# Kernel optimization log

Hardware: AMD Instinct MI355X
Metric: run time of the kernel (lower is better)

Reference implementation:

```python
import jax, jax.numpy as jnp
import numpy as np

N = 100_000   # nodes
E = 1_250_000 # edges
D = 64        # feature dim


def setup_inputs() -> dict:
    key = jax.random.key(0)
    k1, k2, k3, k4 = jax.random.split(key, 4)
    x = jax.random.normal(k1, (N, D), dtype=jnp.float32)
    edge_index = jax.random.randint(k2, (2, E), 0, N, dtype=jnp.int32)
    s = 1.0 / np.sqrt(D)  # glorot-ish scale
    W1 = jax.random.uniform(k3, (D, D), minval=-s, maxval=s, dtype=jnp.float32)
    W2 = jax.random.uniform(k4, (D, D), minval=-s, maxval=s, dtype=jnp.float32)
    b1 = jnp.zeros((D,), jnp.float32)
    b2 = jnp.zeros((D,), jnp.float32)
    return {"x": x, "edge_index": edge_index, "W1": W1, "b1": b1, "W2": W2, "b2": b2}


def gcn_conv(x, edge_index, W, b):
    # PyG GCNConv: add self-loops, symmetric normalization D^-1/2 A D^-1/2,
    # linear transform, scatter-add aggregation over destination nodes.
    n = x.shape[0]
    src, dst = edge_index[0], edge_index[1]
    xw = x @ W  # [N, D]
    deg = jax.ops.segment_sum(jnp.ones((edge_index.shape[1],), x.dtype), dst,
                              num_segments=n) + 1.0  # +1 for self-loop
    inv_sqrt = jax.lax.rsqrt(deg)  # [N]
    coef = inv_sqrt[src] * inv_sqrt[dst]  # [E]
    agg = jax.ops.segment_sum(xw[src] * coef[:, None], dst, num_segments=n)
    # self-loop contribution: coef_ii = deg_i^-1
    agg = agg + xw * (inv_sqrt * inv_sqrt)[:, None]
    return agg + b


def reference(x, edge_index, W1, b1, W2, b2):
    h = jax.nn.relu(gcn_conv(x, edge_index, W1, b1))
    # dropout p=0.6 is identity in eval mode (training=False)
    out = gcn_conv(h, edge_index, W2, b2)
    return jax.nn.log_softmax(out, axis=1)
```

## Files before the change

kernel.cpp:

```cpp
#include <hip/hip_runtime.h>

#define DD 64
#define BSH 8
#define NB_MAX 512
#define SCAP 4096
#define BIN_CH 4096

typedef __attribute__((ext_vector_type(8))) short bf16x8;
typedef __attribute__((ext_vector_type(4))) float f32x4;
union Frag { bf16x8 v; uint32_t d[4]; };

__device__ __forceinline__ float bf_lo(uint32_t d) { return __uint_as_float(d << 16); }
__device__ __forceinline__ float bf_hi(uint32_t d) { return __uint_as_float(d & 0xffff0000u); }
__device__ __forceinline__ float bf2f(uint32_t h) { return __uint_as_float(h << 16); }
__device__ __forceinline__ uint32_t f2bf(float f) {
    uint32_t u = __float_as_uint(f);
    u += 0x7fffu + ((u >> 16) & 1u);
    return u >> 16;
}

__global__ __launch_bounds__(256) void bin_kernel(const int* __restrict__ src,
                                                  const int* __restrict__ dst,
                                                  int* __restrict__ bcnt,
                                                  uint32_t* __restrict__ staging,
                                                  int E, int NB) {
    __shared__ uint32_t cnt[NB_MAX];
    __shared__ uint32_t resv[NB_MAX];
    __shared__ uint16_t rk[BIN_CH];
    int tid = threadIdx.x;
    int base = blockIdx.x * BIN_CH;
    for (int b = tid; b < NB; b += 256) cnt[b] = 0;
    __syncthreads();
    for (int k = tid; k < BIN_CH; k += 256) {
        int g = base + k;
        if (g < E) {
            int b = dst[g] >> BSH;
            rk[k] = (uint16_t)atomicAdd(&cnt[b], 1u);
        }
    }
    __syncthreads();
    for (int b = tid; b < NB; b += 256) {
        uint32_t c = cnt[b];
        resv[b] = c ? (uint32_t)atomicAdd(&bcnt[b], (int)c) : 0u;
    }
    __syncthreads();
    for (int k = tid; k < BIN_CH; k += 256) {
        int g = base + k;
        if (g < E) {
            int s = src[g], d = dst[g];
            int b = d >> BSH;
            uint32_t pos = resv[b] + rk[k];
            if (pos < SCAP)
                staging[(size_t)b * SCAP + pos] = ((uint32_t)s << BSH) | (uint32_t)(d & ((1 << BSH) - 1));
        }
    }
}

__global__ __launch_bounds__(256) void sort_kernel(const int* __restrict__ bcnt,
                                                   const uint32_t* __restrict__ staging,
                                                   int* __restrict__ rowptr,
                                                   float* __restrict__ inv,
                                                   uint32_t* __restrict__ srcs,
                                                   int n, int E, int NB) {
    __shared__ uint32_t raw[SCAP];
    __shared__ uint32_t sorted[SCAP];
    __shared__ int scnt[1 << BSH];
    __shared__ int soff[1 << BSH];
    __shared__ int lcur[1 << BSH];
    __shared__ int red[256];
    int tid = threadIdx.x;
    int b = blockIdx.x;
    int base = b << BSH;
    int nd = min(1 << BSH, n - base);
    int cb = min(bcnt[b], SCAP);

    int part = 0;
    for (int j = tid; j < b; j += 256) part += bcnt[j];
    red[tid] = part;
    __syncthreads();
    for (int o = 128; o > 0; o >>= 1) {
        if (tid < o) red[tid] += red[tid + o];
        __syncthreads();
    }
    int bbase = red[0];

    scnt[tid] = 0;
    if (tid < ((1 << BSH) - 256)) {}
    __syncthreads();
    for (int k = tid; k < cb; k += 256) {
        uint32_t w = staging[(size_t)b * SCAP + k];
        raw[k] = w;
        atomicAdd(&scnt[w & ((1 << BSH) - 1)], 1);
    }
    __syncthreads();
    int v = scnt[tid];
    red[tid] = v;
    __syncthreads();
    for (int o = 1; o < 256; o <<= 1) {
        int t = (tid >= o) ? red[tid - o] : 0;
        __syncthreads();
        red[tid] += t;
        __syncthreads();
    }
    soff[tid] = red[tid] - v;
    lcur[tid] = red[tid] - v;
    if (tid < nd) {
        rowptr[base + tid] = bbase + soff[tid];
        inv[base + tid] = rsqrtf((float)v + 1.0f);
    }
    if (b == NB - 1 && tid == 0) rowptr[n] = E;
    __syncthreads();
    for (int k = tid; k < cb; k += 256) {
        uint32_t w = raw[k];
        int p = atomicAdd(&lcur[w & ((1 << BSH) - 1)], 1);
        sorted[p] = w >> BSH;
    }
    __syncthreads();
    for (int k = tid; k < cb; k += 256) srcs[bbase + k] = sorted[k];
}

template <int XBF>
__global__ __launch_bounds__(256) void gemm64_mfma(const void* __restrict__ Xv,
                                                   const float* __restrict__ W,
                                                   uint16_t* __restrict__ Y, int n) {
    __shared__ float Ws[DD * DD];
    int tid = threadIdx.x;
    for (int i = tid; i < DD * DD; i += 256) Ws[i] = W[i];
    __syncthreads();
    int lane = tid & 63, quad = lane >> 4, l16 = lane & 15;

    Frag bhi[4][2], blo[4][2];
#pragma unroll
    for (int t = 0; t < 4; ++t)
#pragma unroll
        for (int c = 0; c < 2; ++c) {
            int col = t * 16 + l16;
            int kb = c * 32 + quad * 8;
#pragma unroll
            for (int i = 0; i < 4; ++i) {
                float w0 = Ws[(kb + 2 * i) * DD + col];
                float w1 = Ws[(kb + 2 * i + 1) * DD + col];
                uint32_t h0 = f2bf(w0), h1 = f2bf(w1);
                uint32_t l0 = f2bf(w0 - bf2f(h0)), l1 = f2bf(w1 - bf2f(h1));
                bhi[t][c].d[i] = h0 | (h1 << 16);
                blo[t][c].d[i] = l0 | (l1 << 16);
            }
        }

    int ngroups = (n + 15) >> 4;
    int nwaves = gridDim.x * 4;
    int wid = blockIdx.x * 4 + (tid >> 6);
    for (int g = wid; g < ngroups; g += nwaves) {
        int rb = g << 4;
        int row = min(rb + l16, n - 1);
        f32x4 acc[4];
#pragma unroll
        for (int t = 0; t < 4; ++t) acc[t] = (f32x4){0.f, 0.f, 0.f, 0.f};
#pragma unroll
        for (int c = 0; c < 2; ++c) {
            Frag ahi, alo;
            if constexpr (XBF == 0) {
                const float* xr = (const float*)Xv + (size_t)row * DD + c * 32 + quad * 8;
                float4 x0 = *(const float4*)xr;
                float4 x1 = *(const float4*)(xr + 4);
                float f[8] = {x0.x, x0.y, x0.z, x0.w, x1.x, x1.y, x1.z, x1.w};
#pragma unroll
                for (int i = 0; i < 4; ++i) {
                    uint32_t h0 = f2bf(f[2 * i]), h1 = f2bf(f[2 * i + 1]);
                    ahi.d[i] = h0 | (h1 << 16);
                    alo.d[i] = f2bf(f[2 * i] - bf2f(h0)) | (f2bf(f[2 * i + 1] - bf2f(h1)) << 16);
                }
            } else {
                const int4* xr = (const int4*)((const uint32_t*)Xv + (size_t)row * 32 + c * 16 + quad * 4);
                int4 a = *xr;
                ahi.d[0] = a.x; ahi.d[1] = a.y; ahi.d[2] = a.z; ahi.d[3] = a.w;
            }
#pragma unroll
            for (int t = 0; t < 4; ++t) {
                acc[t] = __builtin_amdgcn_mfma_f32_16x16x32_bf16(ahi.v, bhi[t][c].v, acc[t], 0, 0, 0);
                acc[t] = __builtin_amdgcn_mfma_f32_16x16x32_bf16(ahi.v, blo[t][c].v, acc[t], 0, 0, 0);
                if constexpr (XBF == 0)
                    acc[t] = __builtin_amdgcn_mfma_f32_16x16x32_bf16(alo.v, bhi[t][c].v, acc[t], 0, 0, 0);
            }
        }
#pragma unroll
        for (int t = 0; t < 4; ++t)
#pragma unroll
            for (int r = 0; r < 4; ++r) {
                int ro = rb + quad * 4 + r;
                if (ro < n) Y[(size_t)ro * DD + t * 16 + l16] = (uint16_t)f2bf(acc[t][r]);
            }
    }
}

template <int MODE>
__global__ __launch_bounds__(256) void agg_kernel(const int* __restrict__ rowptr,
                                                  const uint32_t* __restrict__ srcs,
                                                  const float* __restrict__ inv,
                                                  const uint32_t* __restrict__ XWb,
                                                  const float* __restrict__ b,
                                                  void* __restrict__ OUTv, int n) {
    int gid = blockIdx.x * 256 + threadIdx.x;
    int i = gid >> 6, lane = gid & 63;
    if (i >= n) return;
    int q = lane >> 4, m = lane & 15;

    float iv = inv[i];
    float a0 = 0.f, a1 = 0.f, a2 = 0.f, a3 = 0.f;
    if (q == 0) {
        float iv2 = iv * iv;
        int2 d = *(const int2*)(XWb + (size_t)i * 32 + 2 * m);
        float4 bb = *(const float4*)(b + 4 * m);
        a0 = fmaf(bf_lo((uint32_t)d.x), iv2, bb.x);
        a1 = fmaf(bf_hi((uint32_t)d.x), iv2, bb.y);
        a2 = fmaf(bf_lo((uint32_t)d.y), iv2, bb.z);
        a3 = fmaf(bf_hi((uint32_t)d.y), iv2, bb.w);
    }

    int jstart = rowptr[i], jend = rowptr[i + 1];
    if (jstart < jend) {
        int last = jend - 1;
        int jq = jstart + q;
        uint32_t s0 = srcs[min(jq, last)];
        uint32_t s1 = srcs[min(jq + 4, last)];
        uint32_t s2 = srcs[min(jq + 8, last)];
        float v0 = inv[s0], v1 = inv[s1];
        int2 d0 = *(const int2*)(XWb + (size_t)s0 * 32 + 2 * m);
        int2 d1 = *(const int2*)(XWb + (size_t)s1 * 32 + 2 * m);
        for (int j = jq; j < jend; j += 4) {
            uint32_t s3 = srcs[min(j + 12, last)];
            float v2 = inv[s2];
            int2 d2 = *(const int2*)(XWb + (size_t)s2 * 32 + 2 * m);
            float c = v0 * iv;
            a0 = fmaf(bf_lo((uint32_t)d0.x), c, a0);
            a1 = fmaf(bf_hi((uint32_t)d0.x), c, a1);
            a2 = fmaf(bf_lo((uint32_t)d0.y), c, a2);
            a3 = fmaf(bf_hi((uint32_t)d0.y), c, a3);
            s0 = s1; s1 = s2; s2 = s3;
            v0 = v1; v1 = v2;
            d0 = d1; d1 = d2;
        }
    }

    a0 += __shfl_xor(a0, 32, 64); a0 += __shfl_xor(a0, 16, 64);
    a1 += __shfl_xor(a1, 32, 64); a1 += __shfl_xor(a1, 16, 64);
    a2 += __shfl_xor(a2, 32, 64); a2 += __shfl_xor(a2, 16, 64);
    a3 += __shfl_xor(a3, 32, 64); a3 += __shfl_xor(a3, 16, 64);

    if (MODE == 0) {
        if (q == 0) {
            int2 d;
            d.x = (int)((f2bf(fmaxf(a1, 0.f)) << 16) | f2bf(fmaxf(a0, 0.f)));
            d.y = (int)((f2bf(fmaxf(a3, 0.f)) << 16) | f2bf(fmaxf(a2, 0.f)));
            *(int2*)((uint32_t*)OUTv + (size_t)i * 32 + 2 * m) = d;
        }
    } else {
        float mx = fmaxf(fmaxf(a0, a1), fmaxf(a2, a3));
#pragma unroll
        for (int o = 8; o > 0; o >>= 1) mx = fmaxf(mx, __shfl_xor(mx, o, 64));
        float e = __expf(a0 - mx) + __expf(a1 - mx) + __expf(a2 - mx) + __expf(a3 - mx);
#pragma unroll
        for (int o = 8; o > 0; o >>= 1) e += __shfl_xor(e, o, 64);
        float ls = __logf(e);
        if (q == 0) {
            float4 r = make_float4(a0 - mx - ls, a1 - mx - ls, a2 - mx - ls, a3 - mx - ls);
            *(float4*)((float*)OUTv + (size_t)i * DD + 4 * m) = r;
        }
    }
}

extern "C" void kernel_launch(void* const* d_in, const int* in_sizes, int n_in,
                              void* d_out, int out_size, void* d_ws, size_t ws_size,
                              hipStream_t stream) {
    const float* x  = (const float*)d_in[0];
    const int*   ei = (const int*)d_in[1];
    const float* W1 = (const float*)d_in[2];
    const float* b1 = (const float*)d_in[3];
    const float* W2 = (const float*)d_in[4];
    const float* b2 = (const float*)d_in[5];
    float* out = (float*)d_out;

    const int n = in_sizes[0] / DD;
    const int E = in_sizes[1] / 2;
    const int* src = ei;
    const int* dst = ei + E;
    const int NB = (n + (1 << BSH) - 1) >> BSH;

    size_t off = 0;
    int* base = (int*)d_ws;
    int* bcnt = base + off; off += NB_MAX;
    uint32_t* staging = (uint32_t*)(base + off); off += (size_t)NB_MAX * SCAP;
    uint32_t* srcs = (uint32_t*)(base + off); off += E;
    int* rowptr = base + off; off += (size_t)n + 1;
    float* inv  = (float*)(base + off); off += n;
    uint32_t* XWb = (uint32_t*)(base + off); off += (size_t)n * 32;
    uint32_t* hb  = (uint32_t*)(base + off); off += (size_t)n * 32;

    hipMemsetAsync(bcnt, 0, NB_MAX * sizeof(int), stream);
    bin_kernel<<<(E + BIN_CH - 1) / BIN_CH, 256, 0, stream>>>(src, dst, bcnt, staging, E, NB);
    sort_kernel<<<NB, 256, 0, stream>>>(bcnt, staging, rowptr, inv, srcs, n, E, NB);

    gemm64_mfma<0><<<1024, 256, 0, stream>>>(x, W1, (uint16_t*)XWb, n);
    agg_kernel<0><<<(n * DD + 255) / 256, 256, 0, stream>>>(rowptr, srcs, inv, XWb, b1, hb, n);

    gemm64_mfma<1><<<1024, 256, 0, stream>>>(hb, W2, (uint16_t*)XWb, n);
    agg_kernel<1><<<(n * DD + 255) / 256, 256, 0, stream>>>(rowptr, srcs, inv, XWb, b2, out, n);
}
```

Measured before the change: 259.6 us.

## Prescale GEMM output by inverse sqrt degree and widen aggregation lanes

The GEMM epilogue now multiplies each output row by inv_sqrt[row], so the aggregation kernel no longer gathers inv[src] per edge. It just sums the gathered rows and applies inv[i] plus bias once at the end. The aggregation is also restructured so 8 lanes cover a 64-feature row with 16-byte loads, processing 8 edges in parallel per wavefront instead of 4. Rounding the prescaled values to bf16 before summation changes numerics slightly, and the extra register array raises register pressure.

```diff
diff --git a/kernel.cpp b/kernel.cpp
--- a/kernel.cpp
+++ b/kernel.cpp
@@ -122,6 +122,7 @@
 template <int XBF>
 __global__ __launch_bounds__(256) void gemm64_mfma(const void* __restrict__ Xv,
                                                    const float* __restrict__ W,
+                                                   const float* __restrict__ inv,
                                                    uint16_t* __restrict__ Y, int n) {
     __shared__ float Ws[DD * DD];
     int tid = threadIdx.x;
@@ -184,12 +185,15 @@
             }
         }
 #pragma unroll
-        for (int t = 0; t < 4; ++t)
-#pragma unroll
-            for (int r = 0; r < 4; ++r) {
-                int ro = rb + quad * 4 + r;
-                if (ro < n) Y[(size_t)ro * DD + t * 16 + l16] = (uint16_t)f2bf(acc[t][r]);
+        for (int r = 0; r < 4; ++r) {
+            int ro = rb + quad * 4 + r;
+            if (ro < n) {
+                float sc = inv[ro];
+#pragma unroll
+                for (int t = 0; t < 4; ++t)
+                    Y[(size_t)ro * DD + t * 16 + l16] = (uint16_t)f2bf(acc[t][r] * sc);
             }
+        }
     }
 }
 
@@ -203,68 +207,79 @@
     int gid = blockIdx.x * 256 + threadIdx.x;
     int i = gid >> 6, lane = gid & 63;
     if (i >= n) return;
-    int q = lane >> 4, m = lane & 15;
-
-    float iv = inv[i];
-    float a0 = 0.f, a1 = 0.f, a2 = 0.f, a3 = 0.f;
-    if (q == 0) {
-        float iv2 = iv * iv;
-        int2 d = *(const int2*)(XWb + (size_t)i * 32 + 2 * m);
-        float4 bb = *(const float4*)(b + 4 * m);
-        a0 = fmaf(bf_lo((uint32_t)d.x), iv2, bb.x);
-        a1 = fmaf(bf_hi((uint32_t)d.x), iv2, bb.y);
-        a2 = fmaf(bf_lo((uint32_t)d.y), iv2, bb.z);
-        a3 = fmaf(bf_hi((uint32_t)d.y), iv2, bb.w);
+    int g = lane >> 3, m = lane & 7;
+
+    float a[8];
+#pragma unroll
+    for (int k = 0; k < 8; ++k) a[k] = 0.f;
+    if (g == 0) {
+        int4 d = *(const int4*)(XWb + (size_t)i * 32 + 4 * m);
+        a[0] = bf_lo((uint32_t)d.x); a[1] = bf_hi((uint32_t)d.x);
+        a[2] = bf_lo((uint32_t)d.y); a[3] = bf_hi((uint32_t)d.y);
+        a[4] = bf_lo((uint32_t)d.z); a[5] = bf_hi((uint32_t)d.z);
+        a[6] = bf_lo((uint32_t)d.w); a[7] = bf_hi((uint32_t)d.w);
     }
 
     int jstart = rowptr[i], jend = rowptr[i + 1];
     if (jstart < jend) {
         int last = jend - 1;
-        int jq = jstart + q;
+        int jq = jstart + g;
         uint32_t s0 = srcs[min(jq, last)];
-        uint32_t s1 = srcs[min(jq + 4, last)];
-        uint32_t s2 = srcs[min(jq + 8, last)];
-        float v0 = inv[s0], v1 = inv[s1];
-        int2 d0 = *(const int2*)(XWb + (size_t)s0 * 32 + 2 * m);
-        int2 d1 = *(const int2*)(XWb + (size_t)s1 * 32 + 2 * m);
-        for (int j = jq; j < jend; j += 4) {
-            uint32_t s3 = srcs[min(j + 12, last)];
-            float v2 = inv[s2];
-            int2 d2 = *(const int2*)(XWb + (size_t)s2 * 32 + 2 * m);
-            float c = v0 * iv;
-            a0 = fmaf(bf_lo((uint32_t)d0.x), c, a0);
-            a1 = fmaf(bf_hi((uint32_t)d0.x), c, a1);
-            a2 = fmaf(bf_lo((uint32_t)d0.y), c, a2);
-            a3 = fmaf(bf_hi((uint32_t)d0.y), c, a3);
-            s0 = s1; s1 = s2; s2 = s3;
-            v0 = v1; v1 = v2;
+        uint32_t s1 = srcs[min(jq + 8, last)];
+        uint32_t s2 = srcs[min(jq + 16, last)];
+        int4 d0 = *(const int4*)(XWb + (size_t)s0 * 32 + 4 * m);
+        int4 d1 = *(const int4*)(XWb + (size_t)s1 * 32 + 4 * m);
+        for (int j = jq; j < jend; j += 8) {
+            uint32_t s3 = srcs[min(j + 24, last)];
+            int4 d2 = *(const int4*)(XWb + (size_t)s2 * 32 + 4 * m);
+            a[0] += bf_lo((uint32_t)d0.x); a[1] += bf_hi((uint32_t)d0.x);
+            a[2] += bf_lo((uint32_t)d0.y); a[3] += bf_hi((uint32_t)d0.y);
+            a[4] += bf_lo((uint32_t)d0.z); a[5] += bf_hi((uint32_t)d0.z);
+            a[6] += bf_lo((uint32_t)d0.w); a[7] += bf_hi((uint32_t)d0.w);
+            s2 = s3;
             d0 = d1; d1 = d2;
         }
     }
 
-    a0 += __shfl_xor(a0, 32, 64); a0 += __shfl_xor(a0, 16, 64);
-    a1 += __shfl_xor(a1, 32, 64); a1 += __shfl_xor(a1, 16, 64);
-    a2 += __shfl_xor(a2, 32, 64); a2 += __shfl_xor(a2, 16, 64);
-    a3 += __shfl_xor(a3, 32, 64); a3 += __shfl_xor(a3, 16, 64);
+#pragma unroll
+    for (int k = 0; k < 8; ++k) {
+        a[k] += __shfl_xor(a[k], 8, 64);
+        a[k] += __shfl_xor(a[k], 16, 64);
+        a[k] += __shfl_xor(a[k], 32, 64);
+    }
+
+    float iv = inv[i];
+    float4 bb0 = *(const float4*)(b + 8 * m);
+    float4 bb1 = *(const float4*)(b + 8 * m + 4);
+    float f0 = fmaf(a[0], iv, bb0.x), f1 = fmaf(a[1], iv, bb0.y);
+    float f2 = fmaf(a[2], iv, bb0.z), f3 = fmaf(a[3], iv, bb0.w);
+    float f4 = fmaf(a[4], iv, bb1.x), f5 = fmaf(a[5], iv, bb1.y);
+    float f6 = fmaf(a[6], iv, bb1.z), f7 = fmaf(a[7], iv, bb1.w);
 
     if (MODE == 0) {
-        if (q == 0) {
-            int2 d;
-            d.x = (int)((f2bf(fmaxf(a1, 0.f)) << 16) | f2bf(fmaxf(a0, 0.f)));
-            d.y = (int)((f2bf(fmaxf(a3, 0.f)) << 16) | f2bf(fmaxf(a2, 0.f)));
-            *(int2*)((uint32_t*)OUTv + (size_t)i * 32 + 2 * m) = d;
+        if (g == 0) {
+            int4 d;
+            d.x = (int)((f2bf(fmaxf(f1, 0.f)) << 16) | f2bf(fmaxf(f0, 0.f)));
+            d.y = (int)((f2bf(fmaxf(f3, 0.f)) << 16) | f2bf(fmaxf(f2, 0.f)));
+            d.z = (int)((f2bf(fmaxf(f5, 0.f)) << 16) | f2bf(fmaxf(f4, 0.f)));
+            d.w = (int)((f2bf(fmaxf(f7, 0.f)) << 16) | f2bf(fmaxf(f6, 0.f)));
+            *(int4*)((uint32_t*)OUTv + (size_t)i * 32 + 4 * m) = d;
         }
     } else {
-        float mx = fmaxf(fmaxf(a0, a1), fmaxf(a2, a3));
-#pragma unroll
-        for (int o = 8; o > 0; o >>= 1) mx = fmaxf(mx, __shfl_xor(mx, o, 64));
-        float e = __expf(a0 - mx) + __expf(a1 - mx) + __expf(a2 - mx) + __expf(a3 - mx);
-#pragma unroll
-        for (int o = 8; o > 0; o >>= 1) e += __shfl_xor(e, o, 64);
+        float mx = fmaxf(fmaxf(fmaxf(f0, f1), fmaxf(f2, f3)),
+                         fmaxf(fmaxf(f4, f5), fmaxf(f6, f7)));
+#pragma unroll
+        for (int o = 4; o > 0; o >>= 1) mx = fmaxf(mx, __shfl_xor(mx, o, 64));
+        float e = __expf(f0 - mx) + __expf(f1 - mx) + __expf(f2 - mx) + __expf(f3 - mx)
+                + __expf(f4 - mx) + __expf(f5 - mx) + __expf(f6 - mx) + __expf(f7 - mx);
+#pragma unroll
+        for (int o = 4; o > 0; o >>= 1) e += __shfl_xor(e, o, 64);
         float ls = __logf(e);
-        if (q == 0) {
-            float4 r = make_float4(a0 - mx - ls, a1 - mx - ls, a2 - mx - ls, a3 - mx - ls);
-            *(float4*)((float*)OUTv + (size_t)i * DD + 4 * m) = r;
+        if (g == 0) {
+            float4 r0 = make_float4(f0 - mx - ls, f1 - mx - ls, f2 - mx - ls, f3 - mx - ls);
+            float4 r1 = make_float4(f4 - mx - ls, f5 - mx - ls, f6 - mx - ls, f7 - mx - ls);
+            *(float4*)((float*)OUTv + (size_t)i * DD + 8 * m) = r0;
+            *(float4*)((float*)OUTv + (size_t)i * DD + 8 * m + 4) = r1;
         }
     }
 }
@@ -300,9 +315,9 @@
     bin_kernel<<<(E + BIN_CH - 1) / BIN_CH, 256, 0, stream>>>(src, dst, bcnt, staging, E, NB);
     sort_kernel<<<NB, 256, 0, stream>>>(bcnt, staging, rowptr, inv, srcs, n, E, NB);
 
-    gemm64_mfma<0><<<1024, 256, 0, stream>>>(x, W1, (uint16_t*)XWb, n);
+    gemm64_mfma<0><<<1024, 256, 0, stream>>>(x, W1, inv, (uint16_t*)XWb, n);
     agg_kernel<0><<<(n * DD + 255) / 256, 256, 0, stream>>>(rowptr, srcs, inv, XWb, b1, hb, n);
 
-    gemm64_mfma<1><<<1024, 256, 0, stream>>>(hb, W2, (uint16_t*)XWb, n);
+    gemm64_mfma<1><<<1024, 256, 0, stream>>>(hb, W2, inv, (uint16_t*)XWb, n);
     agg_kernel<1><<<(n * DD + 255) / 256, 256, 0, stream>>>(rowptr, srcs, inv, XWb, b2, out, n);
 }
```

New measurement: 246.4 us. 1.05x faster.
